# Performance work log

Hardware: AMD Instinct MI355X
Metric: run time of the kernel (lower is better)

Reference implementation:

```python
import jax, jax.numpy as jnp
import numpy as np

N_NODES = 20000
N_REL = 8
N_EDGES = 320000
IN_DIM, HID_DIM, OUT_DIM = 1280, 512, 256


def _rgcn_layer(x, W, root, bias, src, dst, etype):
    """PyG RGCNConv with num_bases=None, aggr='mean' (mean per (node, relation)).
    x: [N, in], W: [R, in, out], root: [in, out], bias: [out].
    """
    n = x.shape[0]
    # per-(dst, relation) in-degree for relation-wise mean
    key = dst * N_REL + etype  # [E]
    counts = jax.ops.segment_sum(jnp.ones(etype.shape, x.dtype), key,
                                 num_segments=n * N_REL)
    deg = jnp.maximum(counts[key], 1.0)  # [E]
    # transform once per relation, then gather per edge
    H = jnp.einsum('ni,rio->rno', x, W)          # [R, N, out]
    msg = H[etype, src] / deg[:, None]           # [E, out]
    agg = jax.ops.segment_sum(msg, dst, num_segments=n)  # [N, out]
    return agg + x @ root + bias


def setup_inputs() -> dict:
    key = jax.random.key(0)
    ks = jax.random.split(key, 9)
    x = jax.random.normal(ks[0], (N_NODES, IN_DIM), dtype=jnp.float32)
    edge_index = jax.random.randint(ks[1], (2, N_EDGES), 0, N_NODES, dtype=jnp.int32)
    edge_type = jax.random.randint(ks[2], (N_EDGES,), 0, N_REL, dtype=jnp.int32)
    s1 = 1.0 / np.sqrt(IN_DIM)
    s2 = 1.0 / np.sqrt(HID_DIM)
    return {
        'x': x,
        'edge_index': edge_index,
        'edge_type': edge_type,
        'W1': jax.random.normal(ks[3], (N_REL, IN_DIM, HID_DIM), dtype=jnp.float32) * s1,
        'root1': jax.random.normal(ks[4], (IN_DIM, HID_DIM), dtype=jnp.float32) * s1,
        'b1': jnp.zeros((HID_DIM,), dtype=jnp.float32),
        'W2': jax.random.normal(ks[5], (N_REL, HID_DIM, OUT_DIM), dtype=jnp.float32) * s2,
        'root2': jax.random.normal(ks[6], (HID_DIM, OUT_DIM), dtype=jnp.float32) * s2,
        'b2': jnp.zeros((OUT_DIM,), dtype=jnp.float32),
    }


def reference(x, edge_index, edge_type, W1, root1, b1, W2, root2, b2):
    src, dst = edge_index[0], edge_index[1]
    h = _rgcn_layer(x, W1, root1, b1, src, dst, edge_type)
    h = jax.nn.relu(h)
    # dropout is identity in eval mode
    out = _rgcn_layer(h, W2, root2, b2, src, dst, edge_type)
    return out
```

## Files before the change

kernel.cpp:

```cpp
#include <hip/hip_runtime.h>
#include <hip/hip_bf16.h>

#define N_REL 8

typedef unsigned short ushort_t;
typedef unsigned int uint_t;
typedef __attribute__((ext_vector_type(8))) short short8;
typedef __attribute__((ext_vector_type(4))) float floatx4;

static __device__ __forceinline__ ushort_t f2bf(float f) {
    union { float f; unsigned u; } v; v.f = f;
    unsigned r = v.u + 0x7fff + ((v.u >> 16) & 1);
    return (ushort_t)(r >> 16);
}

typedef __attribute__((address_space(1))) void glob_void;
typedef __attribute__((address_space(3))) void lds_void;

static __device__ __forceinline__ void load_lds16(const void* g, void* l) {
    __builtin_amdgcn_global_load_lds((glob_void*)g, (lds_void*)l, 16, 0, 0);
}

static __device__ __forceinline__ void stage_half(const ushort_t* __restrict__ g,
                                                  int row0, int rmax, int K, int k0,
                                                  ushort_t* lds, int w, int l) {
    const int rl = l >> 3;
    const int gc = ((l & 7) ^ rl) * 8;
#pragma unroll
    for (int s = 0; s < 2; ++s) {
        int r = row0 + s * 64 + w * 8 + rl;
        r = r < rmax ? r : rmax - 1;
        load_lds16(g + (size_t)r * K + k0 + gc, lds + (s * 64 + w * 8) * 64);
    }
}


__global__ __launch_bounds__(256) void hist_kernel(const int* __restrict__ dst,
                                                   const int* __restrict__ et,
                                                   int* __restrict__ cnt, int E) {
    int e = blockIdx.x * blockDim.x + threadIdx.x;
    if (e < E) atomicAdd(&cnt[dst[e] * N_REL + et[e]], 1);
}

__global__ __launch_bounds__(256) void scan1(const int* __restrict__ cnt,
                                             int* __restrict__ off,
                                             int* __restrict__ bsum, int nk) {
    __shared__ int s[256];
    int t = threadIdx.x;
    int k = blockIdx.x * 256 + t;
    int v = k < nk ? cnt[k] : 0;
    s[t] = v; __syncthreads();
    for (int d = 1; d < 256; d <<= 1) {
        int x = (t >= d) ? s[t - d] : 0;
        __syncthreads(); s[t] += x; __syncthreads();
    }
    if (k < nk) off[k] = s[t] - v;
    if (t == 255) bsum[blockIdx.x] = s[255];
}

__global__ __launch_bounds__(1024) void scan2(int* __restrict__ bsum, int nb) {
    __shared__ int s[1024];
    int t = threadIdx.x;
    int v = t < nb ? bsum[t] : 0;
    s[t] = v; __syncthreads();
    for (int d = 1; d < 1024; d <<= 1) {
        int x = (t >= d) ? s[t - d] : 0;
        __syncthreads(); s[t] += x; __syncthreads();
    }
    if (t < nb) bsum[t] = s[t] - v;
}

__global__ __launch_bounds__(256) void scan3(int* __restrict__ off,
                                             const int* __restrict__ bsum,
                                             int* __restrict__ cursor,
                                             int nk) {
    int k = blockIdx.x * 256 + threadIdx.x;
    if (k >= nk) return;
    int o = off[k] + bsum[k >> 8];
    off[k] = o;
    cursor[k] = o;
}

__global__ __launch_bounds__(256) void scatter_desc(const int* __restrict__ dst,
                                                    const int* __restrict__ et,
                                                    const int* __restrict__ src,
                                                    const int* __restrict__ cnt,
                                                    int* __restrict__ cursor,
                                                    uint2* __restrict__ edesc, int E) {
    int e = blockIdx.x * blockDim.x + threadIdx.x;
    if (e < E) {
        int key = dst[e] * N_REL + et[e];
        int pos = atomicAdd(&cursor[key], 1);
        float inv = 1.0f / (float)cnt[key];
        edesc[pos] = make_uint2((uint_t)src[e] | ((uint_t)et[e] << 27),
                                __float_as_uint(inv));
    }
}


__global__ __launch_bounds__(256) void cast_bf16(const float* __restrict__ in,
                                                 ushort_t* __restrict__ out, long n) {
    long idx = ((long)blockIdx.x * blockDim.x + threadIdx.x) * 4;
    if (idx + 4 <= n) {
        float4 v = *(const float4*)(in + idx);
        ushort_t o[4] = {f2bf(v.x), f2bf(v.y), f2bf(v.z), f2bf(v.w)};
        *(uint2*)(out + idx) = *(const uint2*)o;
    } else {
        for (; idx < n; ++idx) out[idx] = f2bf(in[idx]);
    }
}

__global__ __launch_bounds__(256) void transpose_cast(const float* __restrict__ in,
                                                      ushort_t* __restrict__ out,
                                                      int K, int N) {
    __shared__ float tile[32][33];
    const float* inp = in + (size_t)blockIdx.z * K * N;
    ushort_t* outp = out + (size_t)blockIdx.z * K * N;
    int n0 = blockIdx.x * 32, k0 = blockIdx.y * 32;
    int tx = threadIdx.x & 31, ty = threadIdx.x >> 5;
#pragma unroll
    for (int s = 0; s < 4; ++s)
        tile[ty + 8 * s][tx] = inp[(size_t)(k0 + ty + 8 * s) * N + n0 + tx];
    __syncthreads();
#pragma unroll
    for (int s = 0; s < 4; ++s)
        outp[(size_t)(n0 + ty + 8 * s) * K + k0 + tx] = f2bf(tile[tx][ty + 8 * s]);
}


#define STAGE_A(b, h, ktx) stage_half(A, bm + (h) * 128, M, K, ((ktx) << 6), &sh.st[(b)][0][(h)][0], w, l)
#define STAGE_B(b, h, ktx) stage_half(Bt, bn + (h) * 128, N, K, ((ktx) << 6), &sh.st[(b)][1][(h)][0], w, l)

#define LOAD_A(b, qm)                                                          \
    {                                                                          \
        const ushort_t* pa_ = &sh.st[(b)][0][(qm)][0];                         \
        _Pragma("unroll") for (int i_ = 0; i_ < 4; ++i_) {                     \
            const int r_ = wm * 64 + i_ * 16 + l16;                            \
            _Pragma("unroll") for (int kk_ = 0; kk_ < 2; ++kk_) {              \
                const int ch_ = (kk_ * 4 + quad) ^ (r_ & 7);                   \
                areg[i_][kk_] = *(const short8*)&pa_[r_ * 64 + ch_ * 8];       \
            }                                                                  \
        }                                                                      \
    }

#define LOAD_B(b, qn)                                                          \
    {                                                                          \
        const ushort_t* pb_ = &sh.st[(b)][1][(qn)][0];                         \
        _Pragma("unroll") for (int j_ = 0; j_ < 2; ++j_) {                     \
            const int r_ = wn * 32 + j_ * 16 + l16;                            \
            _Pragma("unroll") for (int kk_ = 0; kk_ < 2; ++kk_) {              \
                const int ch_ = (kk_ * 4 + quad) ^ (r_ & 7);                   \
                breg[(qn)][j_][kk_] = *(const short8*)&pb_[r_ * 64 + ch_ * 8]; \
            }                                                                  \
        }                                                                      \
    }

#define MFMA_Q(qm, qn)                                                              \
    _Pragma("unroll") for (int i_ = 0; i_ < 4; ++i_)                                \
        _Pragma("unroll") for (int j_ = 0; j_ < 2; ++j_)                            \
            _Pragma("unroll") for (int kk_ = 0; kk_ < 2; ++kk_)                     \
                acc[(qm)][(qn)][i_][j_] = __builtin_amdgcn_mfma_f32_16x16x32_bf16(  \
                    areg[i_][kk_], breg[(qn)][j_][kk_], acc[(qm)][(qn)][i_][j_], 0, 0, 0);

#define PHASE_SYNC()                                                           \
    __builtin_amdgcn_s_barrier();                                              \
    asm volatile("s_waitcnt lgkmcnt(0)" ::: "memory");                         \
    __builtin_amdgcn_sched_barrier(0)

#define WINDOW(kt, b)                                                          \
    {                                                                          \
                                 \
        LOAD_A(b, 0);                                                          \
        LOAD_B(b, 0);                                                          \
        if ((kt) + 1 < nkt) STAGE_A((b) ^ 1, 1, (kt) + 1);                     \
        PHASE_SYNC();                                                          \
        __builtin_amdgcn_s_setprio(1);                                         \
        MFMA_Q(0, 0);                                                          \
        __builtin_amdgcn_s_setprio(0);                                         \
        __builtin_amdgcn_s_barrier();                                          \
                        \
        LOAD_B(b, 1);                                                          \
        if ((kt) + 2 < nkt) STAGE_A(b, 0, (kt) + 2);                           \
        PHASE_SYNC();                                                          \
        __builtin_amdgcn_s_setprio(1);                                         \
        MFMA_Q(0, 1);                                                          \
        __builtin_amdgcn_s_setprio(0);                                         \
        __builtin_amdgcn_s_barrier();                                          \
                            \
        LOAD_A(b, 1);                                                          \
        if ((kt) + 2 < nkt) STAGE_B(b, 0, (kt) + 2);                           \
        PHASE_SYNC();                                                          \
        __builtin_amdgcn_s_setprio(1);                                         \
        MFMA_Q(1, 0);                                                          \
        __builtin_amdgcn_s_setprio(0);                                         \
        __builtin_amdgcn_s_barrier();                                          \
           \
        if ((kt) + 2 < nkt) {                                                  \
            STAGE_B(b, 1, (kt) + 2);                                           \
            asm volatile("s_waitcnt vmcnt(6)" ::: "memory");                   \
        } else {                                                               \
            asm volatile("s_waitcnt vmcnt(0)" ::: "memory");   \
        }                                                                      \
        __builtin_amdgcn_s_barrier();                                          \
        __builtin_amdgcn_sched_barrier(0);                                     \
        __builtin_amdgcn_s_setprio(1);                                         \
        MFMA_Q(1, 1);                                                          \
        __builtin_amdgcn_s_setprio(0);                                         \
        __builtin_amdgcn_s_barrier();                                          \
    }

__global__ __launch_bounds__(512, 2) void gemm256p2(const ushort_t* __restrict__ A,
                                                    const ushort_t* __restrict__ Bt,
                                                    ushort_t* __restrict__ C,
                                                    int M, int K, int N,
                                                    int ntiles, int nx) {
    __shared__ struct {
        __align__(16) ushort_t st[2][2][2][128 * 64];
        __align__(16) ushort_t c2[32 * 256];
    } sh;

    const int t = threadIdx.x;
    const int l = t & 63;
    const int w = t >> 6;
    const int wm = w >> 2, wn = w & 3;
    const int quad = l >> 4, l16 = l & 15;

    const int nkt = K >> 6;
    const int q8 = ntiles >> 3, r8 = ntiles & 7;

    int T = blockIdx.x;
    if (T >= ntiles) return;
    int bm, bn, bm2 = 0, bn2 = 0;
    {
        const int xcd = T & 7;
        const int wgid = ((xcd < r8) ? xcd * (q8 + 1) : r8 * (q8 + 1) + (xcd - r8) * q8) + (T >> 3);
        bm = (wgid / nx) * 256;
        bn = (wgid % nx) * 256;
    }

    floatx4 acc[2][2][4][2];
    short8 areg[4][2];
    short8 breg[2][2][2];

    STAGE_A(0, 0, 0); STAGE_B(0, 0, 0); STAGE_B(0, 1, 0); STAGE_A(0, 1, 0);
    STAGE_A(1, 0, 1); STAGE_B(1, 0, 1); STAGE_B(1, 1, 1);
    asm volatile("s_waitcnt vmcnt(6)" ::: "memory");
    __builtin_amdgcn_s_barrier();

    while (true) {
#pragma unroll
        for (int a = 0; a < 2; ++a)
#pragma unroll
            for (int bq = 0; bq < 2; ++bq)
#pragma unroll
                for (int i = 0; i < 4; ++i)
#pragma unroll
                    for (int j = 0; j < 2; ++j) acc[a][bq][i][j] = (floatx4)(0.f);

        for (int kt = 0; kt < nkt; kt += 2) {
            WINDOW(kt, 0);
            WINDOW(kt + 1, 1);
        }

        const int Tn = T + gridDim.x;
        const bool have_next = Tn < ntiles;
        if (have_next) {
            const int xcd = Tn & 7;
            const int wgid = ((xcd < r8) ? xcd * (q8 + 1) : r8 * (q8 + 1) + (xcd - r8) * q8) + (Tn >> 3);
            bm2 = (wgid / nx) * 256;
            bn2 = (wgid % nx) * 256;
            stage_half(A, bm2,       M, K, 0,  &sh.st[0][0][0][0], w, l);
            stage_half(Bt, bn2,      N, K, 0,  &sh.st[0][1][0][0], w, l);
            stage_half(Bt, bn2 + 128, N, K, 0, &sh.st[0][1][1][0], w, l);
            stage_half(A, bm2 + 128, M, K, 0,  &sh.st[0][0][1][0], w, l);
            stage_half(A, bm2,       M, K, 64, &sh.st[1][0][0][0], w, l);
            stage_half(Bt, bn2,      N, K, 64, &sh.st[1][1][0][0], w, l);
            stage_half(Bt, bn2 + 128, N, K, 64, &sh.st[1][1][1][0], w, l);
        }

#pragma unroll
        for (int pc = 0; pc < 8; ++pc) {
            const int qm = pc >> 2;
            const int wmSel = (pc >> 1) & 1;
            const int ih = pc & 1;
            if (wm == wmSel) {
#pragma unroll
                for (int qn = 0; qn < 2; ++qn)
#pragma unroll
                    for (int io = 0; io < 2; ++io)
#pragma unroll
                        for (int j = 0; j < 2; ++j) {
                            const int cl = qn * 128 + wn * 32 + j * 16 + l16;
                            const int i = ih * 2 + io;
#pragma unroll
                            for (int rg = 0; rg < 4; ++rg)
                                sh.c2[(io * 16 + quad * 4 + rg) * 256 + cl] =
                                    f2bf(acc[qm][qn][i][j][rg]);
                        }
            }
            asm volatile("s_waitcnt lgkmcnt(0)" ::: "memory");
            __builtin_amdgcn_s_barrier();
#pragma unroll
            for (int it = 0; it < 2; ++it) {
                const int idx = it * 512 + t;
                const int rl = idx >> 5;
                const int ch8 = (idx & 31) * 8;
                const int grow = bm + pc * 32 + rl;
                if (grow < M)
                    *(uint4*)(C + (size_t)grow * N + bn + ch8) =
                        *(const uint4*)&sh.c2[rl * 256 + ch8];
            }
            __builtin_amdgcn_s_barrier();
        }

        if (!have_next) break;
        T = Tn; bm = bm2; bn = bn2;
        asm volatile("s_waitcnt vmcnt(6)" ::: "memory");
        __builtin_amdgcn_s_barrier();
    }
}

#undef STAGE_A
#undef STAGE_B
#undef LOAD_A
#undef LOAD_B
#undef MFMA_Q
#undef PHASE_SYNC
#undef WINDOW


template <int DIM, bool L1MODE>
__global__ __launch_bounds__(128) void segsum_node(const ushort_t* __restrict__ H,
                                                   const float* __restrict__ bias,
                                                   const int* __restrict__ off,
                                                   const int* __restrict__ cnt,
                                                   const uint2* __restrict__ edesc,
                                                   ushort_t* __restrict__ outb,
                                                   float* __restrict__ outf) {
    constexpr int VPT = DIM / 128;
    constexpr int WPT = VPT / 2;
    const int d = blockIdx.x;
    const int t = threadIdx.x;
    const int hs = (N_REL + 1) * DIM;

    const int base = off[d * N_REL];
    const int total = off[d * N_REL + N_REL - 1] + cnt[d * N_REL + N_REL - 1] - base;

    float acc[VPT];
    {
        uint_t rw[WPT];
        const ushort_t* hp = H + (size_t)d * hs + VPT * t;
        if constexpr (WPT == 2) *(uint2*)rw = *(const uint2*)hp;
        else                    rw[0] = *(const uint_t*)hp;
#pragma unroll
        for (int jq = 0; jq < WPT; ++jq) {
            acc[2 * jq]     = __uint_as_float(rw[jq] << 16);
            acc[2 * jq + 1] = __uint_as_float(rw[jq] & 0xffff0000u);
        }
        const float* bp = bias + VPT * t;
#pragma unroll
        for (int jq = 0; jq < VPT; ++jq) acc[jq] += bp[jq];
    }

    const uint2* __restrict__ ed = edesc + base;
    const ushort_t* __restrict__ Hlane = H + VPT * t;

    for (int p = 0; p < total; p += 8) {
        uint2 dsc[8];
#pragma unroll
        for (int q = 0; q < 8; ++q) {
            const int idx = (p + q < total) ? p + q : total - 1;
            dsc[q] = ed[idx];
        }
#pragma unroll
        for (int q = 0; q < 8; ++q)
            if (p + q >= total) dsc[q].y = 0u;
        uint_t val[8][WPT];
#pragma unroll
        for (int q = 0; q < 8; ++q) {
            const uint_t pk = dsc[q].x;
            const size_t s = pk & 0x07ffffffu;
            const int r = pk >> 27;
            const ushort_t* hp = Hlane + s * hs + (r + 1) * DIM;
            if constexpr (WPT == 2) *(uint2*)val[q] = *(const uint2*)hp;
            else                    val[q][0] = *(const uint_t*)hp;
        }
#pragma unroll
        for (int q = 0; q < 8; ++q) {
            const float inv = __uint_as_float(dsc[q].y);
#pragma unroll
            for (int jq = 0; jq < WPT; ++jq) {
                acc[2 * jq]     += inv * __uint_as_float(val[q][jq] << 16);
                acc[2 * jq + 1] += inv * __uint_as_float(val[q][jq] & 0xffff0000u);
            }
        }
    }

    if constexpr (L1MODE) {
        ushort_t ob[VPT];
#pragma unroll
        for (int jq = 0; jq < VPT; ++jq) ob[jq] = f2bf(fmaxf(acc[jq], 0.f));
        if constexpr (WPT == 2)
            *(uint2*)(outb + (size_t)d * DIM + VPT * t) = *(const uint2*)ob;
        else
            *(uint_t*)(outb + (size_t)d * DIM + VPT * t) = *(const uint_t*)ob;
    } else {
        float* op = outf + (size_t)d * DIM + VPT * t;
#pragma unroll
        for (int jq = 0; jq < WPT; ++jq)
            *(float2*)(op + 2 * jq) = make_float2(acc[2 * jq], acc[2 * jq + 1]);
    }
}


extern "C" void kernel_launch(void* const* d_in, const int* in_sizes, int n_in,
                              void* d_out, int out_size, void* d_ws, size_t ws_size,
                              hipStream_t stream) {
    const float* x     = (const float*)d_in[0];
    const int*   eidx  = (const int*)d_in[1];
    const int*   etype = (const int*)d_in[2];
    const float* W1    = (const float*)d_in[3];
    const float* root1 = (const float*)d_in[4];
    const float* b1    = (const float*)d_in[5];
    const float* W2    = (const float*)d_in[6];
    const float* root2 = (const float*)d_in[7];
    const float* b2    = (const float*)d_in[8];
    float* out = (float*)d_out;

    const int IN_DIM = 1280, HID_DIM = 512, OUT_DIM = 256;
    const int E = in_sizes[2];
    const int N = in_sizes[0] / IN_DIM;
    const int NK = N * N_REL;
    const int* srcs = eidx;
    const int* dsts = eidx + E;

    char* ws = (char*)d_ws;
    size_t offb = 0;
    auto alloc = [&](size_t bytes) { void* p = ws + offb; offb += (bytes + 255) & ~(size_t)255; return p; };
    int*      cnt    = (int*)alloc((size_t)NK * 4);
    int*      off    = (int*)alloc((size_t)NK * 4);
    int*      cursor = (int*)alloc((size_t)NK * 4);
    int*      bsum   = (int*)alloc(1024 * 4);
    uint2*    edesc  = (uint2*)alloc((size_t)E * 8);
    ushort_t* x_bf   = (ushort_t*)alloc((size_t)N * IN_DIM * 2);
    ushort_t* rW1t   = (ushort_t*)alloc((size_t)(N_REL + 1) * IN_DIM * HID_DIM * 2);
    ushort_t* r1t    = rW1t;
    ushort_t* W1t    = rW1t + (size_t)HID_DIM * IN_DIM;
    ushort_t* rW2t   = (ushort_t*)alloc((size_t)(N_REL + 1) * HID_DIM * OUT_DIM * 2);
    ushort_t* r2t    = rW2t;
    ushort_t* W2t    = rW2t + (size_t)OUT_DIM * HID_DIM;
    ushort_t* Hb     = (ushort_t*)alloc((size_t)N * (N_REL + 1) * HID_DIM * 2);
    ushort_t* hb_bf  = x_bf;
    (void)ws_size;

    const int nb = (NK + 255) / 256;

    hipMemsetAsync(cnt, 0, (size_t)NK * 4, stream);
    hist_kernel<<<(E + 255) / 256, 256, 0, stream>>>(dsts, etype, cnt, E);
    scan1<<<nb, 256, 0, stream>>>(cnt, off, bsum, NK);
    scan2<<<1, 1024, 0, stream>>>(bsum, nb);
    scan3<<<nb, 256, 0, stream>>>(off, bsum, cursor, NK);
    scatter_desc<<<(E + 255) / 256, 256, 0, stream>>>(dsts, etype, srcs, cnt, cursor, edesc, E);

    {
        long n = (long)N * IN_DIM;
        cast_bf16<<<(unsigned)((n / 4 + 255) / 256), 256, 0, stream>>>(x, x_bf, n);
    }
    transpose_cast<<<dim3(HID_DIM / 32, IN_DIM / 32, 1), 256, 0, stream>>>(root1, r1t, IN_DIM, HID_DIM);
    transpose_cast<<<dim3(HID_DIM / 32, IN_DIM / 32, N_REL), 256, 0, stream>>>(W1, W1t, IN_DIM, HID_DIM);
    transpose_cast<<<dim3(OUT_DIM / 32, HID_DIM / 32, 1), 256, 0, stream>>>(root2, r2t, HID_DIM, OUT_DIM);
    transpose_cast<<<dim3(OUT_DIM / 32, HID_DIM / 32, N_REL), 256, 0, stream>>>(W2, W2t, HID_DIM, OUT_DIM);

    const int mb = (N + 255) / 256;

    {
        const int NTOT = (N_REL + 1) * HID_DIM;
        const int nxg = NTOT / 256;
        gemm256p2<<<256, 512, 0, stream>>>(x_bf, rW1t, Hb, N, IN_DIM, NTOT, mb * nxg, nxg);
        segsum_node<512, true><<<N, 128, 0, stream>>>(Hb, b1, off, cnt, edesc, hb_bf, nullptr);
    }

    {
        const int NTOT = (N_REL + 1) * OUT_DIM;
        const int nxg = NTOT / 256;
        gemm256p2<<<256, 512, 0, stream>>>(hb_bf, rW2t, Hb, N, HID_DIM, NTOT, mb * nxg, nxg);
        segsum_node<256, false><<<N, 128, 0, stream>>>(Hb, b2, off, cnt, edesc, nullptr, out);
    }
}
```

Before: 621.2 us.

## Overlap next-tile prologue staging with last K-windows and use single-wave segment sums

The persistent GEMM no longer stages the next tile's first two K-slices after the main loop. It peels the last two windows into special variants that issue those loads in between the MFMA phases, which hides the prologue latency behind compute. The per-window bound checks are removed from the steady-state loop. The segment-sum kernel now uses one 64-lane wave per node with wider vector loads and an exact tail loop instead of padded batches. This risks correctness if nkt is odd or below 4, and it gives fewer threads per node for latency hiding.

```diff
diff --git a/kernel.cpp b/kernel.cpp
--- a/kernel.cpp
+++ b/kernel.cpp
@@ -167,40 +167,27 @@
     asm volatile("s_waitcnt lgkmcnt(0)" ::: "memory");                         \
     __builtin_amdgcn_sched_barrier(0)
 
+#define MFMA_PHASE(qm, qn)                                                     \
+    PHASE_SYNC();                                                              \
+    __builtin_amdgcn_s_setprio(1);                                             \
+    MFMA_Q(qm, qn);                                                            \
+    __builtin_amdgcn_s_setprio(0);                                             \
+    __builtin_amdgcn_s_barrier()
+
 #define WINDOW(kt, b)                                                          \
     {                                                                          \
-                                 \
         LOAD_A(b, 0);                                                          \
         LOAD_B(b, 0);                                                          \
-        if ((kt) + 1 < nkt) STAGE_A((b) ^ 1, 1, (kt) + 1);                     \
-        PHASE_SYNC();                                                          \
-        __builtin_amdgcn_s_setprio(1);                                         \
-        MFMA_Q(0, 0);                                                          \
-        __builtin_amdgcn_s_setprio(0);                                         \
-        __builtin_amdgcn_s_barrier();                                          \
-                        \
+        STAGE_A((b) ^ 1, 1, (kt) + 1);                                         \
+        MFMA_PHASE(0, 0);                                                      \
         LOAD_B(b, 1);                                                          \
-        if ((kt) + 2 < nkt) STAGE_A(b, 0, (kt) + 2);                           \
-        PHASE_SYNC();                                                          \
-        __builtin_amdgcn_s_setprio(1);                                         \
-        MFMA_Q(0, 1);                                                          \
-        __builtin_amdgcn_s_setprio(0);                                         \
-        __builtin_amdgcn_s_barrier();                                          \
-                            \
+        STAGE_A(b, 0, (kt) + 2);                                               \
+        MFMA_PHASE(0, 1);                                                      \
         LOAD_A(b, 1);                                                          \
-        if ((kt) + 2 < nkt) STAGE_B(b, 0, (kt) + 2);                           \
-        PHASE_SYNC();                                                          \
-        __builtin_amdgcn_s_setprio(1);                                         \
-        MFMA_Q(1, 0);                                                          \
-        __builtin_amdgcn_s_setprio(0);                                         \
-        __builtin_amdgcn_s_barrier();                                          \
-           \
-        if ((kt) + 2 < nkt) {                                                  \
-            STAGE_B(b, 1, (kt) + 2);                                           \
-            asm volatile("s_waitcnt vmcnt(6)" ::: "memory");                   \
-        } else {                                                               \
-            asm volatile("s_waitcnt vmcnt(0)" ::: "memory");   \
-        }                                                                      \
+        STAGE_B(b, 0, (kt) + 2);                                               \
+        MFMA_PHASE(1, 0);                                                      \
+        STAGE_B(b, 1, (kt) + 2);                                               \
+        asm volatile("s_waitcnt vmcnt(6)" ::: "memory");                       \
         __builtin_amdgcn_s_barrier();                                          \
         __builtin_amdgcn_sched_barrier(0);                                     \
         __builtin_amdgcn_s_setprio(1);                                         \
@@ -209,11 +196,55 @@
         __builtin_amdgcn_s_barrier();                                          \
     }
 
-__global__ __launch_bounds__(512, 2) void gemm256p2(const ushort_t* __restrict__ A,
-                                                    const ushort_t* __restrict__ Bt,
-                                                    ushort_t* __restrict__ C,
-                                                    int M, int K, int N,
-                                                    int ntiles, int nx) {
+#define WINDOW_S0()                                                            \
+    {                                                                          \
+        LOAD_A(0, 0);                                                          \
+        LOAD_B(0, 0);                                                          \
+        STAGE_A(1, 1, nkt - 1);                                                \
+        MFMA_PHASE(0, 0);                                                      \
+        LOAD_B(0, 1);                                                          \
+        stage_half(A, bm2, M, K, 0, &sh.st[0][0][0][0], w, l);                 \
+        MFMA_PHASE(0, 1);                                                      \
+        LOAD_A(0, 1);                                                          \
+        stage_half(Bt, bn2, N, K, 0, &sh.st[0][1][0][0], w, l);                \
+        MFMA_PHASE(1, 0);                                                      \
+        stage_half(Bt, bn2 + 128, N, K, 0, &sh.st[0][1][1][0], w, l);          \
+        asm volatile("s_waitcnt vmcnt(6)" ::: "memory");                       \
+        __builtin_amdgcn_s_barrier();                                          \
+        __builtin_amdgcn_sched_barrier(0);                                     \
+        __builtin_amdgcn_s_setprio(1);                                         \
+        MFMA_Q(1, 1);                                                          \
+        __builtin_amdgcn_s_setprio(0);                                         \
+        __builtin_amdgcn_s_barrier();                                          \
+    }
+
+#define WINDOW_S1()                                                            \
+    {                                                                          \
+        LOAD_A(1, 0);                                                          \
+        LOAD_B(1, 0);                                                          \
+        stage_half(A, bm2 + 128, M, K, 0, &sh.st[0][0][1][0], w, l);           \
+        MFMA_PHASE(0, 0);                                                      \
+        LOAD_B(1, 1);                                                          \
+        stage_half(A, bm2, M, K, 64, &sh.st[1][0][0][0], w, l);                \
+        MFMA_PHASE(0, 1);                                                      \
+        LOAD_A(1, 1);                                                          \
+        stage_half(Bt, bn2, N, K, 64, &sh.st[1][1][0][0], w, l);               \
+        MFMA_PHASE(1, 0);                                                      \
+        stage_half(Bt, bn2 + 128, N, K, 64, &sh.st[1][1][1][0], w, l);         \
+        asm volatile("s_waitcnt vmcnt(6)" ::: "memory");                       \
+        __builtin_amdgcn_s_barrier();                                          \
+        __builtin_amdgcn_sched_barrier(0);                                     \
+        __builtin_amdgcn_s_setprio(1);                                         \
+        MFMA_Q(1, 1);                                                          \
+        __builtin_amdgcn_s_setprio(0);                                         \
+        __builtin_amdgcn_s_barrier();                                          \
+    }
+
+__global__ __launch_bounds__(512, 2) void gemm256s(const ushort_t* __restrict__ A,
+                                                   const ushort_t* __restrict__ Bt,
+                                                   ushort_t* __restrict__ C,
+                                                   int M, int K, int N,
+                                                   int ntiles, int nx) {
     __shared__ struct {
         __align__(16) ushort_t st[2][2][2][128 * 64];
         __align__(16) ushort_t c2[32 * 256];
@@ -230,13 +261,23 @@
 
     int T = blockIdx.x;
     if (T >= ntiles) return;
-    int bm, bn, bm2 = 0, bn2 = 0;
+    int bm, bn, bm2, bn2;
     {
         const int xcd = T & 7;
         const int wgid = ((xcd < r8) ? xcd * (q8 + 1) : r8 * (q8 + 1) + (xcd - r8) * q8) + (T >> 3);
         bm = (wgid / nx) * 256;
         bn = (wgid % nx) * 256;
     }
+    int Tn = T + gridDim.x;
+    bool have_next = Tn < ntiles;
+    if (have_next) {
+        const int xcd = Tn & 7;
+        const int wgid = ((xcd < r8) ? xcd * (q8 + 1) : r8 * (q8 + 1) + (xcd - r8) * q8) + (Tn >> 3);
+        bm2 = (wgid / nx) * 256;
+        bn2 = (wgid % nx) * 256;
+    } else {
+        bm2 = bm; bn2 = bn;
+    }
 
     floatx4 acc[2][2][4][2];
     short8 areg[4][2];
@@ -257,26 +298,12 @@
 #pragma unroll
                     for (int j = 0; j < 2; ++j) acc[a][bq][i][j] = (floatx4)(0.f);
 
-        for (int kt = 0; kt < nkt; kt += 2) {
+        for (int kt = 0; kt + 3 < nkt; kt += 2) {
             WINDOW(kt, 0);
             WINDOW(kt + 1, 1);
         }
-
-        const int Tn = T + gridDim.x;
-        const bool have_next = Tn < ntiles;
-        if (have_next) {
-            const int xcd = Tn & 7;
-            const int wgid = ((xcd < r8) ? xcd * (q8 + 1) : r8 * (q8 + 1) + (xcd - r8) * q8) + (Tn >> 3);
-            bm2 = (wgid / nx) * 256;
-            bn2 = (wgid % nx) * 256;
-            stage_half(A, bm2,       M, K, 0,  &sh.st[0][0][0][0], w, l);
-            stage_half(Bt, bn2,      N, K, 0,  &sh.st[0][1][0][0], w, l);
-            stage_half(Bt, bn2 + 128, N, K, 0, &sh.st[0][1][1][0], w, l);
-            stage_half(A, bm2 + 128, M, K, 0,  &sh.st[0][0][1][0], w, l);
-            stage_half(A, bm2,       M, K, 64, &sh.st[1][0][0][0], w, l);
-            stage_half(Bt, bn2,      N, K, 64, &sh.st[1][1][0][0], w, l);
-            stage_half(Bt, bn2 + 128, N, K, 64, &sh.st[1][1][1][0], w, l);
-        }
+        WINDOW_S0();
+        WINDOW_S1();
 
 #pragma unroll
         for (int pc = 0; pc < 8; ++pc) {
@@ -313,10 +340,21 @@
             __builtin_amdgcn_s_barrier();
         }
 
-        if (!have_next) break;
+        if (!have_next) {
+            asm volatile("s_waitcnt vmcnt(0)" ::: "memory");
+            break;
+        }
         T = Tn; bm = bm2; bn = bn2;
-        asm volatile("s_waitcnt vmcnt(6)" ::: "memory");
-        __builtin_amdgcn_s_barrier();
+        Tn += gridDim.x;
+        have_next = Tn < ntiles;
+        if (have_next) {
+            const int xcd = Tn & 7;
+            const int wgid = ((xcd < r8) ? xcd * (q8 + 1) : r8 * (q8 + 1) + (xcd - r8) * q8) + (Tn >> 3);
+            bm2 = (wgid / nx) * 256;
+            bn2 = (wgid % nx) * 256;
+        } else {
+            bm2 = bm; bn2 = bn;
+        }
     }
 }
 
@@ -326,18 +364,21 @@
 #undef LOAD_B
 #undef MFMA_Q
 #undef PHASE_SYNC
+#undef MFMA_PHASE
 #undef WINDOW
+#undef WINDOW_S0
+#undef WINDOW_S1
 
 
 template <int DIM, bool L1MODE>
-__global__ __launch_bounds__(128) void segsum_node(const ushort_t* __restrict__ H,
-                                                   const float* __restrict__ bias,
-                                                   const int* __restrict__ off,
-                                                   const int* __restrict__ cnt,
-                                                   const uint2* __restrict__ edesc,
-                                                   ushort_t* __restrict__ outb,
-                                                   float* __restrict__ outf) {
-    constexpr int VPT = DIM / 128;
+__global__ __launch_bounds__(64) void segsum_wave(const ushort_t* __restrict__ H,
+                                                  const float* __restrict__ bias,
+                                                  const int* __restrict__ off,
+                                                  const int* __restrict__ cnt,
+                                                  const uint2* __restrict__ edesc,
+                                                  ushort_t* __restrict__ outb,
+                                                  float* __restrict__ outf) {
+    constexpr int VPT = DIM / 64;
     constexpr int WPT = VPT / 2;
     const int d = blockIdx.x;
     const int t = threadIdx.x;
@@ -350,8 +391,8 @@
     {
         uint_t rw[WPT];
         const ushort_t* hp = H + (size_t)d * hs + VPT * t;
-        if constexpr (WPT == 2) *(uint2*)rw = *(const uint2*)hp;
-        else                    rw[0] = *(const uint_t*)hp;
+        if constexpr (WPT == 4) *(uint4*)rw = *(const uint4*)hp;
+        else                    *(uint2*)rw = *(const uint2*)hp;
 #pragma unroll
         for (int jq = 0; jq < WPT; ++jq) {
             acc[2 * jq]     = __uint_as_float(rw[jq] << 16);
@@ -365,16 +406,11 @@
     const uint2* __restrict__ ed = edesc + base;
     const ushort_t* __restrict__ Hlane = H + VPT * t;
 
-    for (int p = 0; p < total; p += 8) {
+    int p = 0;
+    while (p + 8 <= total) {
         uint2 dsc[8];
 #pragma unroll
-        for (int q = 0; q < 8; ++q) {
-            const int idx = (p + q < total) ? p + q : total - 1;
-            dsc[q] = ed[idx];
-        }
-#pragma unroll
-        for (int q = 0; q < 8; ++q)
-            if (p + q >= total) dsc[q].y = 0u;
+        for (int q = 0; q < 8; ++q) dsc[q] = ed[p + q];
         uint_t val[8][WPT];
 #pragma unroll
         for (int q = 0; q < 8; ++q) {
@@ -382,8 +418,8 @@
             const size_t s = pk & 0x07ffffffu;
             const int r = pk >> 27;
             const ushort_t* hp = Hlane + s * hs + (r + 1) * DIM;
-            if constexpr (WPT == 2) *(uint2*)val[q] = *(const uint2*)hp;
-            else                    val[q][0] = *(const uint_t*)hp;
+            if constexpr (WPT == 4) *(uint4*)val[q] = *(const uint4*)hp;
+            else                    *(uint2*)val[q] = *(const uint2*)hp;
         }
 #pragma unroll
         for (int q = 0; q < 8; ++q) {
@@ -394,16 +430,33 @@
                 acc[2 * jq + 1] += inv * __uint_as_float(val[q][jq] & 0xffff0000u);
             }
         }
+        p += 8;
+    }
+    for (; p < total; ++p) {
+        const uint2 dq = ed[p];
+        const uint_t pk = dq.x;
+        const size_t s = pk & 0x07ffffffu;
+        const int r = pk >> 27;
+        const float inv = __uint_as_float(dq.y);
+        uint_t vw[WPT];
+        const ushort_t* hp = Hlane + s * hs + (r + 1) * DIM;
+        if constexpr (WPT == 4) *(uint4*)vw = *(const uint4*)hp;
+        else                    *(uint2*)vw = *(const uint2*)hp;
+#pragma unroll
+        for (int jq = 0; jq < WPT; ++jq) {
+            acc[2 * jq]     += inv * __uint_as_float(vw[jq] << 16);
+            acc[2 * jq + 1] += inv * __uint_as_float(vw[jq] & 0xffff0000u);
+        }
     }
 
     if constexpr (L1MODE) {
         ushort_t ob[VPT];
 #pragma unroll
         for (int jq = 0; jq < VPT; ++jq) ob[jq] = f2bf(fmaxf(acc[jq], 0.f));
-        if constexpr (WPT == 2)
+        if constexpr (WPT == 4)
+            *(uint4*)(outb + (size_t)d * DIM + VPT * t) = *(const uint4*)ob;
+        else
             *(uint2*)(outb + (size_t)d * DIM + VPT * t) = *(const uint2*)ob;
-        else
-            *(uint_t*)(outb + (size_t)d * DIM + VPT * t) = *(const uint_t*)ob;
     } else {
         float* op = outf + (size_t)d * DIM + VPT * t;
 #pragma unroll
@@ -476,14 +529,14 @@
     {
         const int NTOT = (N_REL + 1) * HID_DIM;
         const int nxg = NTOT / 256;
-        gemm256p2<<<256, 512, 0, stream>>>(x_bf, rW1t, Hb, N, IN_DIM, NTOT, mb * nxg, nxg);
-        segsum_node<512, true><<<N, 128, 0, stream>>>(Hb, b1, off, cnt, edesc, hb_bf, nullptr);
+        gemm256s<<<256, 512, 0, stream>>>(x_bf, rW1t, Hb, N, IN_DIM, NTOT, mb * nxg, nxg);
+        segsum_wave<512, true><<<N, 64, 0, stream>>>(Hb, b1, off, cnt, edesc, hb_bf, nullptr);
     }
 
     {
         const int NTOT = (N_REL + 1) * OUT_DIM;
         const int nxg = NTOT / 256;
-        gemm256p2<<<256, 512, 0, stream>>>(hb_bf, rW2t, Hb, N, HID_DIM, NTOT, mb * nxg, nxg);
-        segsum_node<256, false><<<N, 128, 0, stream>>>(Hb, b2, off, cnt, edesc, nullptr, out);
-    }
-}
+        gemm256s<<<256, 512, 0, stream>>>(hb_bf, rW2t, Hb, N, HID_DIM, NTOT, mb * nxg, nxg);
+        segsum_wave<256, false><<<N, 64, 0, stream>>>(Hb, b2, off, cnt, edesc, nullptr, out);
+    }
+}
```

Measured after the change: 799.6 us. 1.29x slower.
